# Optimization experiments

Measured on AMD Instinct MI355X. Metric: run time of the kernel, lower is better.

Reference implementation:

```python
import jax, jax.numpy as jnp
import numpy as np

N = 65536        # number of encoding vectors (flattened tokens)
K = 1024         # num_embeddings (codebook size)
D = 128          # embedding_dim
BETA = 0.25


def setup_inputs() -> dict:
    key = jax.random.key(0)
    k_enc, k_cb = jax.random.split(key)
    encoding = jax.random.normal(k_enc, (N, D), dtype=jnp.float32)
    # nn.Embedding weight initialized uniform(-1/K, 1/K)
    codebook = jax.random.uniform(k_cb, (K, D), dtype=jnp.float32,
                                  minval=-1.0 / K, maxval=1.0 / K)
    return {"encoding": encoding, "codebook": codebook}


def reference(encoding, codebook):
    # Nearest codebook entry per row. argmin of L2 distance == argmin of
    # squared distance; expand ||e - w||^2 = ||e||^2 - 2 e.w + ||w||^2.
    # ||e||^2 is constant per row, so it does not affect the argmin.
    scores = (-2.0 * jnp.einsum('nd,kd->nk', encoding, codebook)
              + jnp.sum(codebook * codebook, axis=-1)[None, :])  # [N, K]
    quantized_index = jnp.argmin(scores, axis=-1)                # [N] int
    quantized_embedding = codebook[quantized_index]              # [N, D] gather == onehot @ W

    sg = jax.lax.stop_gradient
    commitment_loss = jnp.mean((sg(quantized_embedding) - encoding) ** 2)
    embedding_loss = jnp.mean((quantized_embedding - sg(encoding)) ** 2)
    vq_loss = commitment_loss * BETA + embedding_loss

    # straight-through estimator
    quantized_st = encoding + sg(quantized_embedding - encoding)

    quantized_index = quantized_index[:, None]  # match torch unsqueeze(1) -> [N, 1]
    return (quantized_index, quantized_st, vq_loss, embedding_loss, commitment_loss)
```

## Files before the change

### kernel.cpp

```cpp
#include <hip/hip_runtime.h>


#define NROWS 65536
#define KCB   1024
#define DIM   128
#define DV    32
#define MSE_DENOM 8388608.0f
#define MARGIN 2.0e-5f
#define FLAGCAP 16384
#define CSCALE   1024.0f
#define CDESCALE 0.0009765625f

#define WS_CNORM_F 256
#define WS_LIST_B  8192
#define WS_PH_B    73728
#define WS_NEEDED  335872

typedef __attribute__((ext_vector_type(16))) float float16v;
typedef _Float16 half8 __attribute__((ext_vector_type(8)));
union U4H8 { uint4 u; half8 h; };
union F4A  { float4 v; float f[4]; };
union HU   { _Float16 f; unsigned short u; };

__device__ __forceinline__ unsigned umn(unsigned a, unsigned b) { return a < b ? a : b; }
__device__ __forceinline__ unsigned umx(unsigned a, unsigned b) { return a > b ? a : b; }
__device__ __forceinline__ float unmap_score(unsigned up) {
  return (up & 0x80000000u) ? __uint_as_float(up ^ 0x80000000u) : __uint_as_float(~up);
}
__device__ __forceinline__ void gload16(const void* g, void* s) {
  __builtin_amdgcn_global_load_lds((const __attribute__((address_space(1))) unsigned int*)g,
                                   (__attribute__((address_space(3))) unsigned int*)s,
                                   16, 0, 0);
}

__global__ __launch_bounds__(256) void vq_prep0(const float* __restrict__ C,
                                                float* __restrict__ wsf) {
  int k = blockIdx.x * 256 + threadIdx.x;
  if (k == 0) { wsf[0] = 0.0f; ((unsigned*)wsf)[1] = 0u; }
  const float4* c4 = (const float4*)C + (size_t)k * DV;
  float s = 0.f;
#pragma unroll 8
  for (int i = 0; i < DV; ++i) {
    float4 v = c4[i];
    s = fmaf(v.x, v.x, s); s = fmaf(v.y, v.y, s);
    s = fmaf(v.z, v.z, s); s = fmaf(v.w, v.w, s);
  }
  wsf[WS_CNORM_F + k] = s;
}

__global__ __launch_bounds__(256) void vq_pack(const float* __restrict__ C,
                                               uint4* __restrict__ PH) {
  int g = blockIdx.x * 256 + threadIdx.x;
  int mt = g >> 9, s = (g >> 6) & 7, l = g & 63;
  int cw = mt * 32 + (l & 31);
  int k0 = s * 16 + (l >> 5) * 8;
  const float* src = C + (size_t)cw * DIM + k0;
  float4 x0 = *(const float4*)src;
  float4 x1 = *(const float4*)(src + 4);
  unsigned h[8];
  {
    float v[8] = {x0.x, x0.y, x0.z, x0.w, x1.x, x1.y, x1.z, x1.w};
#pragma unroll
    for (int j = 0; j < 8; ++j) { HU u; u.f = (_Float16)(CSCALE * v[j]); h[j] = u.u; }
  }
  PH[g] = make_uint4(h[0] | (h[1] << 16), h[2] | (h[3] << 16),
                     h[4] | (h[5] << 16), h[6] | (h[7] << 16));
}

__global__ __launch_bounds__(128, 2) void vq_main5(const float* __restrict__ E,
                                                   const float* __restrict__ C,
                                                   float* __restrict__ wsf,
                                                   float* __restrict__ out) {
  __shared__ uint4 SH[2][512];
  __shared__ __align__(16) float CN[1024];
  __shared__ int BI[64];

  const int tid  = threadIdx.x;
  const int w    = tid >> 6;
  const int l    = tid & 63;
  const int half = l >> 5;
  const int rr   = l & 31;
  const int row0 = blockIdx.x * 64;

  const uint4* PHg = (const uint4*)((const char*)wsf + WS_PH_B);

  {
    const uint4* sh = PHg + tid;
    gload16(sh,       &SH[0][0] + tid);
    gload16(sh + 128, &SH[0][0] + tid + 128);
    gload16(sh + 256, &SH[0][0] + tid + 256);
    gload16(sh + 384, &SH[0][0] + tid + 384);
    const uint4* cn = ((const uint4*)(wsf + WS_CNORM_F)) + tid;
    gload16(cn,       ((uint4*)CN) + tid);
    gload16(cn + 128, ((uint4*)CN) + tid + 128);
  }

  half8 beh[8], bel[8];
  float s2 = 0.f;
  const float* erow = E + (size_t)(row0 + w * 32 + rr) * DIM + half * 8;
#pragma unroll
  for (int s = 0; s < 8; ++s) {
    float4 x0 = *(const float4*)(erow + s * 16);
    float4 x1 = *(const float4*)(erow + s * 16 + 4);
    float v[8] = {x0.x, x0.y, x0.z, x0.w, x1.x, x1.y, x1.z, x1.w};
#pragma unroll
    for (int j = 0; j < 8; ++j) {
      float y = v[j];
      s2 = fmaf(y, y, s2);
      float t = -2.f * y;
      _Float16 hh = (_Float16)t;
      beh[s][j] = hh;
      bel[s][j] = (_Float16)(t - (float)hh);
    }
  }

  asm volatile("s_waitcnt vmcnt(0)" ::: "memory");
  __syncthreads();

  unsigned best = 0xFFFFFFFFu, second = 0xFFFFFFFFu;
  float sc[16];
  int tprev = 0;

#define STAGE_TILE(tn)                                                     \
  {                                                                        \
    const uint4* sh_ = PHg + (size_t)(tn) * 512 + tid;                     \
    uint4* dh_ = &SH[(tn) & 1][0];                                         \
    gload16(sh_,       dh_ + tid);                                         \
    gload16(sh_ + 128, dh_ + tid + 128);                                   \
    gload16(sh_ + 256, dh_ + tid + 256);                                   \
    gload16(sh_ + 384, dh_ + tid + 384);                                   \
  }

#define COMPUTE_TILE(tt, A0, A1)                                           \
  _Pragma("unroll")                                                        \
  for (int s = 0; s < 8; s += 2) {                                         \
    U4H8 h0, h1;                                                           \
    h0.u = SH[(tt) & 1][s * 64 + l];                                       \
    h1.u = SH[(tt) & 1][(s + 1) * 64 + l];                                 \
    A0 = __builtin_amdgcn_mfma_f32_32x32x16_f16(h0.h, beh[s],     A0, 0, 0, 0); \
    A1 = __builtin_amdgcn_mfma_f32_32x32x16_f16(h1.h, beh[s + 1], A1, 0, 0, 0); \
    A0 = __builtin_amdgcn_mfma_f32_32x32x16_f16(h0.h, bel[s],     A0, 0, 0, 0); \
    A1 = __builtin_amdgcn_mfma_f32_32x32x16_f16(h1.h, bel[s + 1], A1, 0, 0, 0); \
  }

#define FOLD_PREV()                                                        \
  {                                                                        \
    const unsigned cwb_ = (unsigned)(tprev * 32 + half * 4);               \
    _Pragma("unroll")                                                      \
    for (int q = 0; q < 4; ++q) {                                          \
      F4A a_; a_.v = *(const float4*)&CN[tprev * 32 + q * 8 + half * 4];   \
      _Pragma("unroll")                                                    \
      for (int i = 0; i < 4; ++i) {                                        \
        float scv_ = fmaf(sc[q * 4 + i], CDESCALE, a_.f[i]);               \
        unsigned u_ = __float_as_uint(scv_);                               \
        u_ ^= ((unsigned)(((int)u_) >> 31)) | 0x80000000u;                 \
        u_ = (u_ & 0xFFFFFC00u) | (cwb_ + (unsigned)(q * 8 + i));          \
        unsigned nb_ = umn(best, u_);                                      \
        second = umn(second, umx(best, u_));                               \
        best = nb_;                                                        \
      }                                                                    \
    }                                                                      \
  }

  {
    STAGE_TILE(1);
    float16v acc0 = {0,0,0,0,0,0,0,0,0,0,0,0,0,0,0,0};
    float16v acc1 = {0,0,0,0,0,0,0,0,0,0,0,0,0,0,0,0};
    COMPUTE_TILE(0, acc0, acc1);
#pragma unroll
    for (int r = 0; r < 16; ++r) sc[r] = acc0[r] + acc1[r];
    tprev = 0;
    asm volatile("s_waitcnt vmcnt(0)" ::: "memory");
    __syncthreads();
  }

  for (int t = 1; t < 32; ++t) {
    if (t < 31) STAGE_TILE(t + 1);
    float16v acc0 = {0,0,0,0,0,0,0,0,0,0,0,0,0,0,0,0};
    float16v acc1 = {0,0,0,0,0,0,0,0,0,0,0,0,0,0,0,0};
    COMPUTE_TILE(t, acc0, acc1);
    FOLD_PREV();
#pragma unroll
    for (int r = 0; r < 16; ++r) sc[r] = acc0[r] + acc1[r];
    tprev = t;
    asm volatile("s_waitcnt vmcnt(0)" ::: "memory");
    __syncthreads();
  }
  FOLD_PREV();

  unsigned ob = (unsigned)__shfl_xor((int)best, 32, 64);
  unsigned os = (unsigned)__shfl_xor((int)second, 32, 64);
  unsigned ns = umn(umn(second, os), umx(best, ob));
  unsigned nb = umn(best, ob);
  float en = s2 + __shfl_xor(s2, 32, 64);

  if (half == 0) {
    const int r = w * 32 + rr;
    int   bi = (int)(nb & 1023u);
    float bv = unmap_score(nb & 0xFFFFFC00u);
    float sv = unmap_score(ns & 0xFFFFFC00u);
    out[row0 + r] = (float)bi;
    BI[r] = bi;
    if (sv - bv < MARGIN) {
      unsigned idx = atomicAdd((unsigned*)wsf + 1, 1u);
      if (idx < FLAGCAP) ((int*)((char*)wsf + WS_LIST_B))[idx] = row0 + r;
    }
    float term = en + bv;
#pragma unroll
    for (int off = 16; off > 0; off >>= 1) term += __shfl_down(term, off);
    if (rr == 0) atomicAdd(wsf, term);
  }
  __syncthreads();

  const float4* C4   = (const float4*)C;
  float4*       out4 = (float4*)out;
#pragma unroll
  for (int it = 0; it < 16; ++it) {
    int flat = it * 128 + tid;
    int r = flat >> 5, d4 = flat & 31;
    out4[(NROWS / 4) + (size_t)(row0 + r) * DV + d4] = C4[(size_t)BI[r] * DV + d4];
  }
#undef STAGE_TILE
#undef COMPUTE_TILE
#undef FOLD_PREV
}

__global__ __launch_bounds__(256) void vq_fix(const float* __restrict__ E,
                                              const float* __restrict__ C,
                                              float* __restrict__ wsf,
                                              float* __restrict__ out) {
  __shared__ float4 eL0[32], eL1[32];
  __shared__ float  sv0[256], sv1[256];
  __shared__ int    si0[256], si1[256];
  __shared__ int    RESi[2];
  const int tid = threadIdx.x;
  const int* list = (const int*)((const char*)wsf + WS_LIST_B);
  int nf = (int)((const unsigned*)wsf)[1];
  if (nf > FLAGCAP) nf = FLAGCAP;
  const float4* E4 = (const float4*)E;
  const float4* C4 = (const float4*)C;
  const float*  cn = wsf + WS_CNORM_F;
  float4* out4 = (float4*)out;

  for (int pair = blockIdx.x; pair * 2 < nf; pair += gridDim.x) {
    const int r0 = list[pair * 2];
    const int r1 = (pair * 2 + 1 < nf) ? list[pair * 2 + 1] : r0;
    if (tid < 32) eL0[tid] = E4[(size_t)r0 * DV + tid];
    else if (tid < 64) eL1[tid - 32] = E4[(size_t)r1 * DV + (tid - 32)];
    __syncthreads();
    float bv0 = 3.0e38f, bv1 = 3.0e38f; int bi0 = 0, bi1 = 0;
#pragma unroll
    for (int j = 0; j < 4; ++j) {
      int k = j * 256 + tid;
      float d0 = 0.f, d1 = 0.f;
#pragma unroll 8
      for (int d4 = 0; d4 < 32; ++d4) {
        float4 c = C4[(size_t)k * DV + d4];
        float4 e0 = eL0[d4], e1 = eL1[d4];
        d0 = fmaf(c.x, e0.x, d0); d0 = fmaf(c.y, e0.y, d0);
        d0 = fmaf(c.z, e0.z, d0); d0 = fmaf(c.w, e0.w, d0);
        d1 = fmaf(c.x, e1.x, d1); d1 = fmaf(c.y, e1.y, d1);
        d1 = fmaf(c.z, e1.z, d1); d1 = fmaf(c.w, e1.w, d1);
      }
      float s0 = fmaf(-2.f, d0, cn[k]);
      float s1 = fmaf(-2.f, d1, cn[k]);
      if (s0 < bv0 || (s0 == bv0 && k < bi0)) { bv0 = s0; bi0 = k; }
      if (s1 < bv1 || (s1 == bv1 && k < bi1)) { bv1 = s1; bi1 = k; }
    }
    sv0[tid] = bv0; si0[tid] = bi0; sv1[tid] = bv1; si1[tid] = bi1;
    __syncthreads();
    if (tid < 64) {
      float v0 = sv0[tid]; int i0 = si0[tid];
      float v1 = sv1[tid]; int i1 = si1[tid];
#pragma unroll
      for (int q = 1; q < 4; ++q) {
        float w0 = sv0[tid + q * 64]; int j0 = si0[tid + q * 64];
        float w1 = sv1[tid + q * 64]; int j1 = si1[tid + q * 64];
        if (w0 < v0 || (w0 == v0 && j0 < i0)) { v0 = w0; i0 = j0; }
        if (w1 < v1 || (w1 == v1 && j1 < i1)) { v1 = w1; i1 = j1; }
      }
#pragma unroll
      for (int off = 32; off > 0; off >>= 1) {
        float w0 = __shfl_down(v0, off); int j0 = __shfl_down(i0, off);
        float w1 = __shfl_down(v1, off); int j1 = __shfl_down(i1, off);
        if (w0 < v0 || (w0 == v0 && j0 < i0)) { v0 = w0; i0 = j0; }
        if (w1 < v1 || (w1 == v1 && j1 < i1)) { v1 = w1; i1 = j1; }
      }
      if (tid == 0) {
        RESi[0] = i0; RESi[1] = i1;
        out[r0] = (float)i0; out[r1] = (float)i1;
      }
    }
    __syncthreads();
    if (tid < 32) out4[(NROWS / 4) + (size_t)r0 * DV + tid] = C4[(size_t)RESi[0] * DV + tid];
    else if (tid < 64) out4[(NROWS / 4) + (size_t)r1 * DV + (tid - 32)] = C4[(size_t)RESi[1] * DV + (tid - 32)];
    __syncthreads();
  }
}

__global__ void vq_final(const float* __restrict__ wsf, float* __restrict__ out) {
  if (threadIdx.x == 0 && blockIdx.x == 0) {
    float mse = wsf[0] / MSE_DENOM;
    out[NROWS + NROWS * DIM + 0] = 1.25f * mse;
    out[NROWS + NROWS * DIM + 1] = mse;
    out[NROWS + NROWS * DIM + 2] = mse;
  }
}

__global__ __launch_bounds__(256) void vq_prep_fb(const float* __restrict__ C,
                                                  float* __restrict__ ws) {
  int k = blockIdx.x * 256 + threadIdx.x;
  if (k == 0) ws[0] = 0.0f;
  const float4* c4 = (const float4*)C + (size_t)k * DV;
  float s = 0.f;
#pragma unroll 8
  for (int i = 0; i < DV; ++i) {
    float4 v = c4[i];
    s = fmaf(v.x, v.x, s); s = fmaf(v.y, v.y, s);
    s = fmaf(v.z, v.z, s); s = fmaf(v.w, v.w, s);
  }
  ws[64 + k] = s;
}

__global__ __launch_bounds__(256) void vq_main_fb(const float* __restrict__ E,
                                                  const float* __restrict__ C,
                                                  const float* __restrict__ cnorm,
                                                  float* __restrict__ out,
                                                  float* __restrict__ lossacc) {
  __shared__ float smem[16384];
  float4* EsV = (float4*)smem;
  float4* CsV = (float4*)(smem + 8192);
  const int tid  = threadIdx.x;
  const int row0 = blockIdx.x * 64;
#pragma unroll
  for (int i = 0; i < 8; ++i) {
    int flat = i * 256 + tid;
    int r = flat >> 5, d4 = flat & 31;
    EsV[r * 32 + (d4 ^ (r & 31))] = ((const float4*)E)[(size_t)(row0 + r) * DV + d4];
  }
  const int tx = tid & 15, ty = tid >> 4;
  int rbase[4], rmask[4];
#pragma unroll
  for (int i = 0; i < 4; ++i) { int r = i * 16 + ty; rbase[i] = r * 32; rmask[i] = r & 31; }
  float bestv[4]; int besti[4];
#pragma unroll
  for (int i = 0; i < 4; ++i) { bestv[i] = 3.0e38f; besti[i] = 0; }
  for (int ch = 0; ch < 16; ++ch) {
    const int k0 = ch * 64;
    __syncthreads();
#pragma unroll
    for (int i = 0; i < 8; ++i) {
      int flat = i * 256 + tid;
      int k = flat >> 5, d4 = flat & 31;
      CsV[k * 32 + (d4 ^ (k & 31))] = ((const float4*)C)[(size_t)(k0 + k) * DV + d4];
    }
    __syncthreads();
    float acc[4][4] = {};
#pragma unroll 8
    for (int d4 = 0; d4 < DV; ++d4) {
      float4 a[4], b[4];
#pragma unroll
      for (int i = 0; i < 4; ++i) a[i] = EsV[rbase[i] + (d4 ^ rmask[i])];
#pragma unroll
      for (int j = 0; j < 4; ++j) { int k = j * 16 + tx; b[j] = CsV[k * 32 + (d4 ^ (k & 31))]; }
#pragma unroll
      for (int i = 0; i < 4; ++i)
#pragma unroll
        for (int j = 0; j < 4; ++j) {
          acc[i][j] = fmaf(a[i].x, b[j].x, acc[i][j]);
          acc[i][j] = fmaf(a[i].y, b[j].y, acc[i][j]);
          acc[i][j] = fmaf(a[i].z, b[j].z, acc[i][j]);
          acc[i][j] = fmaf(a[i].w, b[j].w, acc[i][j]);
        }
    }
#pragma unroll
    for (int j = 0; j < 4; ++j) {
      int kg = k0 + j * 16 + tx;
      float cnv = cnorm[kg];
#pragma unroll
      for (int i = 0; i < 4; ++i) {
        float s = fmaf(-2.0f, acc[i][j], cnv);
        if (s < bestv[i] || (s == bestv[i] && kg < besti[i])) { bestv[i] = s; besti[i] = kg; }
      }
    }
  }
  float* Rv = smem + 8192;
  int*   Ri = (int*)(smem + 9216);
  int*   BIf = (int*)(smem + 10240);
  __syncthreads();
#pragma unroll
  for (int i = 0; i < 4; ++i) {
    int r = i * 16 + ty;
    Rv[r * 16 + tx] = bestv[i];
    Ri[r * 16 + tx] = besti[i];
  }
  __syncthreads();
  if (tid < 64) {
    const int r = tid;
    float bv = Rv[r * 16]; int bi = Ri[r * 16];
#pragma unroll
    for (int t = 1; t < 16; ++t) {
      float v = Rv[r * 16 + t]; int ii = Ri[r * 16 + t];
      if (v < bv || (v == bv && ii < bi)) { bv = v; bi = ii; }
    }
    float en = 0.f;
#pragma unroll 8
    for (int d4 = 0; d4 < DV; ++d4) {
      float4 v = EsV[r * 32 + (d4 ^ (r & 31))];
      en = fmaf(v.x, v.x, en); en = fmaf(v.y, v.y, en);
      en = fmaf(v.z, v.z, en); en = fmaf(v.w, v.w, en);
    }
    out[row0 + r] = (float)bi;
    BIf[r] = bi;
    float blocksum = en + bv;
#pragma unroll
    for (int off = 32; off > 0; off >>= 1) blocksum += __shfl_down(blocksum, off);
    if (tid == 0) atomicAdd(lossacc, blocksum);
  }
  __syncthreads();
  const float4* C4   = (const float4*)C;
  float4*       out4 = (float4*)out;
  for (int flat = tid; flat < 64 * DV; flat += 256) {
    int r = flat >> 5, d4 = flat & 31;
    out4[(NROWS / 4) + (size_t)(row0 + r) * DV + d4] = C4[(size_t)BIf[r] * DV + d4];
  }
}

__global__ void vq_final_fb(const float* __restrict__ ws, float* __restrict__ out) {
  if (threadIdx.x == 0 && blockIdx.x == 0) {
    float mse = ws[0] / MSE_DENOM;
    out[NROWS + NROWS * DIM + 0] = 1.25f * mse;
    out[NROWS + NROWS * DIM + 1] = mse;
    out[NROWS + NROWS * DIM + 2] = mse;
  }
}

extern "C" void kernel_launch(void* const* d_in, const int* in_sizes, int n_in,
                              void* d_out, int out_size, void* d_ws, size_t ws_size,
                              hipStream_t stream) {
  const float* E = (const float*)d_in[0];
  const float* C = (const float*)d_in[1];
  float* out = (float*)d_out;
  float* wsf = (float*)d_ws;

  if (ws_size >= (size_t)WS_NEEDED) {
    uint4* PH = (uint4*)((char*)d_ws + WS_PH_B);
    vq_prep0<<<4, 256, 0, stream>>>(C, wsf);
    vq_pack<<<64, 256, 0, stream>>>(C, PH);
    vq_main5<<<NROWS / 64, 128, 0, stream>>>(E, C, wsf, out);
    vq_fix<<<512, 256, 0, stream>>>(E, C, wsf, out);
    vq_final<<<1, 64, 0, stream>>>(wsf, out);
  } else {
    vq_prep_fb<<<4, 256, 0, stream>>>(C, wsf);
    vq_main_fb<<<NROWS / 64, 256, 0, stream>>>(E, C, wsf + 64, out, wsf);
    vq_final_fb<<<1, 64, 0, stream>>>(wsf, out);
  }
}
```

Measured before the change: 167.0 us.

## Drop fp16 lo-split MFMA pass, double tile width, batch four rows in fix

The main kernel now converts the encoding to a single fp16 term instead of a hi+lo split, which halves the number of MFMA instructions. It also stages two 32-codeword tiles per iteration, so there are half as many barriers and fold phases, but the previous fold-overlap pipelining is gone. To make up for the lower precision, the candidate margin widens, and the exact fp32 fix kernel processes four flagged rows per block with wave-level shuffle reductions. The risk is that more rows get flagged for the slower exact fallback pass.

```diff
diff --git a/kernel.cpp b/kernel.cpp
--- a/kernel.cpp
+++ b/kernel.cpp
@@ -6,7 +6,7 @@
 #define DIM   128
 #define DV    32
 #define MSE_DENOM 8388608.0f
-#define MARGIN 2.0e-5f
+#define MARGIN 3.0e-5f
 #define FLAGCAP 16384
 #define CSCALE   1024.0f
 #define CDESCALE 0.0009765625f
@@ -33,9 +33,9 @@
                                    16, 0, 0);
 }
 
-__global__ __launch_bounds__(256) void vq_prep0(const float* __restrict__ C,
-                                                float* __restrict__ wsf) {
-  int k = blockIdx.x * 256 + threadIdx.x;
+__global__ __launch_bounds__(64) void vq_prep0(const float* __restrict__ C,
+                                               float* __restrict__ wsf) {
+  int k = blockIdx.x * 64 + threadIdx.x;
   if (k == 0) { wsf[0] = 0.0f; ((unsigned*)wsf)[1] = 0u; }
   const float4* c4 = (const float4*)C + (size_t)k * DV;
   float s = 0.f;
@@ -67,11 +67,11 @@
                      h[4] | (h[5] << 16), h[6] | (h[7] << 16));
 }
 
-__global__ __launch_bounds__(128, 2) void vq_main5(const float* __restrict__ E,
+__global__ __launch_bounds__(128, 2) void vq_main6(const float* __restrict__ E,
                                                    const float* __restrict__ C,
                                                    float* __restrict__ wsf,
                                                    float* __restrict__ out) {
-  __shared__ uint4 SH[2][512];
+  __shared__ uint4 SH[2][1024];
   __shared__ __align__(16) float CN[1024];
   __shared__ int BI[64];
 
@@ -86,16 +86,15 @@
 
   {
     const uint4* sh = PHg + tid;
-    gload16(sh,       &SH[0][0] + tid);
-    gload16(sh + 128, &SH[0][0] + tid + 128);
-    gload16(sh + 256, &SH[0][0] + tid + 256);
-    gload16(sh + 384, &SH[0][0] + tid + 384);
+#pragma unroll
+    for (int k = 0; k < 8; ++k)
+      gload16(sh + k * 128, &SH[0][0] + tid + k * 128);
     const uint4* cn = ((const uint4*)(wsf + WS_CNORM_F)) + tid;
     gload16(cn,       ((uint4*)CN) + tid);
     gload16(cn + 128, ((uint4*)CN) + tid + 128);
   }
 
-  half8 beh[8], bel[8];
+  half8 beh[8];
   float s2 = 0.f;
   const float* erow = E + (size_t)(row0 + w * 32 + rr) * DIM + half * 8;
 #pragma unroll
@@ -107,10 +106,7 @@
     for (int j = 0; j < 8; ++j) {
       float y = v[j];
       s2 = fmaf(y, y, s2);
-      float t = -2.f * y;
-      _Float16 hh = (_Float16)t;
-      beh[s][j] = hh;
-      bel[s][j] = (_Float16)(t - (float)hh);
+      beh[s][j] = (_Float16)(-2.f * y);
     }
   }
 
@@ -118,75 +114,59 @@
   __syncthreads();
 
   unsigned best = 0xFFFFFFFFu, second = 0xFFFFFFFFu;
-  float sc[16];
-  int tprev = 0;
-
-#define STAGE_TILE(tn)                                                     \
-  {                                                                        \
-    const uint4* sh_ = PHg + (size_t)(tn) * 512 + tid;                     \
-    uint4* dh_ = &SH[(tn) & 1][0];                                         \
-    gload16(sh_,       dh_ + tid);                                         \
-    gload16(sh_ + 128, dh_ + tid + 128);                                   \
-    gload16(sh_ + 256, dh_ + tid + 256);                                   \
-    gload16(sh_ + 384, dh_ + tid + 384);                                   \
-  }
-
-#define COMPUTE_TILE(tt, A0, A1)                                           \
-  _Pragma("unroll")                                                        \
-  for (int s = 0; s < 8; s += 2) {                                         \
-    U4H8 h0, h1;                                                           \
-    h0.u = SH[(tt) & 1][s * 64 + l];                                       \
-    h1.u = SH[(tt) & 1][(s + 1) * 64 + l];                                 \
-    A0 = __builtin_amdgcn_mfma_f32_32x32x16_f16(h0.h, beh[s],     A0, 0, 0, 0); \
-    A1 = __builtin_amdgcn_mfma_f32_32x32x16_f16(h1.h, beh[s + 1], A1, 0, 0, 0); \
-    A0 = __builtin_amdgcn_mfma_f32_32x32x16_f16(h0.h, bel[s],     A0, 0, 0, 0); \
-    A1 = __builtin_amdgcn_mfma_f32_32x32x16_f16(h1.h, bel[s + 1], A1, 0, 0, 0); \
-  }
-
-#define FOLD_PREV()                                                        \
-  {                                                                        \
-    const unsigned cwb_ = (unsigned)(tprev * 32 + half * 4);               \
-    _Pragma("unroll")                                                      \
-    for (int q = 0; q < 4; ++q) {                                          \
-      F4A a_; a_.v = *(const float4*)&CN[tprev * 32 + q * 8 + half * 4];   \
-      _Pragma("unroll")                                                    \
-      for (int i = 0; i < 4; ++i) {                                        \
-        float scv_ = fmaf(sc[q * 4 + i], CDESCALE, a_.f[i]);               \
-        unsigned u_ = __float_as_uint(scv_);                               \
-        u_ ^= ((unsigned)(((int)u_) >> 31)) | 0x80000000u;                 \
-        u_ = (u_ & 0xFFFFFC00u) | (cwb_ + (unsigned)(q * 8 + i));          \
-        unsigned nb_ = umn(best, u_);                                      \
-        second = umn(second, umx(best, u_));                               \
-        best = nb_;                                                        \
-      }                                                                    \
-    }                                                                      \
-  }
-
-  {
-    STAGE_TILE(1);
-    float16v acc0 = {0,0,0,0,0,0,0,0,0,0,0,0,0,0,0,0};
-    float16v acc1 = {0,0,0,0,0,0,0,0,0,0,0,0,0,0,0,0};
-    COMPUTE_TILE(0, acc0, acc1);
-#pragma unroll
-    for (int r = 0; r < 16; ++r) sc[r] = acc0[r] + acc1[r];
-    tprev = 0;
+
+  for (int t = 0; t < 16; ++t) {
+    const int b = t & 1;
+    if (t < 15) {
+      const uint4* sh = PHg + (size_t)(t + 1) * 1024 + tid;
+      uint4* dh = &SH[b ^ 1][0];
+#pragma unroll
+      for (int k = 0; k < 8; ++k)
+        gload16(sh + k * 128, dh + tid + k * 128);
+    }
+
+    float16v a0 = {0,0,0,0,0,0,0,0,0,0,0,0,0,0,0,0};
+    float16v a1 = {0,0,0,0,0,0,0,0,0,0,0,0,0,0,0,0};
+    float16v b0 = {0,0,0,0,0,0,0,0,0,0,0,0,0,0,0,0};
+    float16v b1 = {0,0,0,0,0,0,0,0,0,0,0,0,0,0,0,0};
+#pragma unroll
+    for (int s = 0; s < 8; s += 2) {
+      U4H8 hA0, hA1, hB0, hB1;
+      hA0.u = SH[b][s * 64 + l];
+      hA1.u = SH[b][(s + 1) * 64 + l];
+      hB0.u = SH[b][512 + s * 64 + l];
+      hB1.u = SH[b][512 + (s + 1) * 64 + l];
+      a0 = __builtin_amdgcn_mfma_f32_32x32x16_f16(hA0.h, beh[s],     a0, 0, 0, 0);
+      a1 = __builtin_amdgcn_mfma_f32_32x32x16_f16(hA1.h, beh[s + 1], a1, 0, 0, 0);
+      b0 = __builtin_amdgcn_mfma_f32_32x32x16_f16(hB0.h, beh[s],     b0, 0, 0, 0);
+      b1 = __builtin_amdgcn_mfma_f32_32x32x16_f16(hB1.h, beh[s + 1], b1, 0, 0, 0);
+    }
+
+#pragma unroll
+    for (int tt = 0; tt < 2; ++tt) {
+      const int tg = t * 2 + tt;
+      const unsigned cwb = (unsigned)(tg * 32 + half * 4);
+#pragma unroll
+      for (int q = 0; q < 4; ++q) {
+        F4A a; a.v = *(const float4*)&CN[tg * 32 + q * 8 + half * 4];
+#pragma unroll
+        for (int i = 0; i < 4; ++i) {
+          float acc = tt ? (b0[q * 4 + i] + b1[q * 4 + i])
+                         : (a0[q * 4 + i] + a1[q * 4 + i]);
+          float sc = fmaf(acc, CDESCALE, a.f[i]);
+          unsigned u = __float_as_uint(sc);
+          u ^= ((unsigned)(((int)u) >> 31)) | 0x80000000u;
+          u = (u & 0xFFFFFC00u) | (cwb + (unsigned)(q * 8 + i));
+          unsigned nb = umn(best, u);
+          second = umn(second, umx(best, u));
+          best = nb;
+        }
+      }
+    }
+
     asm volatile("s_waitcnt vmcnt(0)" ::: "memory");
     __syncthreads();
   }
-
-  for (int t = 1; t < 32; ++t) {
-    if (t < 31) STAGE_TILE(t + 1);
-    float16v acc0 = {0,0,0,0,0,0,0,0,0,0,0,0,0,0,0,0};
-    float16v acc1 = {0,0,0,0,0,0,0,0,0,0,0,0,0,0,0,0};
-    COMPUTE_TILE(t, acc0, acc1);
-    FOLD_PREV();
-#pragma unroll
-    for (int r = 0; r < 16; ++r) sc[r] = acc0[r] + acc1[r];
-    tprev = t;
-    asm volatile("s_waitcnt vmcnt(0)" ::: "memory");
-    __syncthreads();
-  }
-  FOLD_PREV();
 
   unsigned ob = (unsigned)__shfl_xor((int)best, 32, 64);
   unsigned os = (unsigned)__shfl_xor((int)second, 32, 64);
@@ -220,20 +200,19 @@
     int r = flat >> 5, d4 = flat & 31;
     out4[(NROWS / 4) + (size_t)(row0 + r) * DV + d4] = C4[(size_t)BI[r] * DV + d4];
   }
-#undef STAGE_TILE
-#undef COMPUTE_TILE
-#undef FOLD_PREV
 }
 
 __global__ __launch_bounds__(256) void vq_fix(const float* __restrict__ E,
                                               const float* __restrict__ C,
                                               float* __restrict__ wsf,
                                               float* __restrict__ out) {
-  __shared__ float4 eL0[32], eL1[32];
-  __shared__ float  sv0[256], sv1[256];
-  __shared__ int    si0[256], si1[256];
-  __shared__ int    RESi[2];
+  __shared__ float4 eL[4][32];
+  __shared__ float  RV[4][4];
+  __shared__ int    RI[4][4];
+  __shared__ int    RESi[4];
   const int tid = threadIdx.x;
+  const int wv  = tid >> 6;
+  const int ln  = tid & 63;
   const int* list = (const int*)((const char*)wsf + WS_LIST_B);
   int nf = (int)((const unsigned*)wsf)[1];
   if (nf > FLAGCAP) nf = FLAGCAP;
@@ -242,58 +221,75 @@
   const float*  cn = wsf + WS_CNORM_F;
   float4* out4 = (float4*)out;
 
-  for (int pair = blockIdx.x; pair * 2 < nf; pair += gridDim.x) {
-    const int r0 = list[pair * 2];
-    const int r1 = (pair * 2 + 1 < nf) ? list[pair * 2 + 1] : r0;
-    if (tid < 32) eL0[tid] = E4[(size_t)r0 * DV + tid];
-    else if (tid < 64) eL1[tid - 32] = E4[(size_t)r1 * DV + (tid - 32)];
-    __syncthreads();
-    float bv0 = 3.0e38f, bv1 = 3.0e38f; int bi0 = 0, bi1 = 0;
+  for (int g = blockIdx.x; g * 4 < nf; g += gridDim.x) {
+    const int base = g * 4;
+    if (tid < 128) {
+      int r = tid >> 5, d4 = tid & 31;
+      int R = (base + r < nf) ? list[base + r] : list[base];
+      eL[r][d4] = E4[(size_t)R * DV + d4];
+    }
+    __syncthreads();
+    float bv[4] = {3.0e38f, 3.0e38f, 3.0e38f, 3.0e38f};
+    int   bi[4] = {0, 0, 0, 0};
 #pragma unroll
     for (int j = 0; j < 4; ++j) {
       int k = j * 256 + tid;
-      float d0 = 0.f, d1 = 0.f;
-#pragma unroll 8
+      float d0 = 0.f, d1 = 0.f, d2 = 0.f, d3 = 0.f;
+#pragma unroll 4
       for (int d4 = 0; d4 < 32; ++d4) {
         float4 c = C4[(size_t)k * DV + d4];
-        float4 e0 = eL0[d4], e1 = eL1[d4];
+        float4 e0 = eL[0][d4], e1 = eL[1][d4], e2 = eL[2][d4], e3 = eL[3][d4];
         d0 = fmaf(c.x, e0.x, d0); d0 = fmaf(c.y, e0.y, d0);
         d0 = fmaf(c.z, e0.z, d0); d0 = fmaf(c.w, e0.w, d0);
         d1 = fmaf(c.x, e1.x, d1); d1 = fmaf(c.y, e1.y, d1);
         d1 = fmaf(c.z, e1.z, d1); d1 = fmaf(c.w, e1.w, d1);
-      }
-      float s0 = fmaf(-2.f, d0, cn[k]);
-      float s1 = fmaf(-2.f, d1, cn[k]);
-      if (s0 < bv0 || (s0 == bv0 && k < bi0)) { bv0 = s0; bi0 = k; }
-      if (s1 < bv1 || (s1 == bv1 && k < bi1)) { bv1 = s1; bi1 = k; }
-    }
-    sv0[tid] = bv0; si0[tid] = bi0; sv1[tid] = bv1; si1[tid] = bi1;
-    __syncthreads();
-    if (tid < 64) {
-      float v0 = sv0[tid]; int i0 = si0[tid];
-      float v1 = sv1[tid]; int i1 = si1[tid];
+        d2 = fmaf(c.x, e2.x, d2); d2 = fmaf(c.y, e2.y, d2);
+        d2 = fmaf(c.z, e2.z, d2); d2 = fmaf(c.w, e2.w, d2);
+        d3 = fmaf(c.x, e3.x, d3); d3 = fmaf(c.y, e3.y, d3);
+        d3 = fmaf(c.z, e3.z, d3); d3 = fmaf(c.w, e3.w, d3);
+      }
+      float cnk = cn[k];
+      float s0 = fmaf(-2.f, d0, cnk);
+      float s1 = fmaf(-2.f, d1, cnk);
+      float s2 = fmaf(-2.f, d2, cnk);
+      float s3 = fmaf(-2.f, d3, cnk);
+      if (s0 < bv[0] || (s0 == bv[0] && k < bi[0])) { bv[0] = s0; bi[0] = k; }
+      if (s1 < bv[1] || (s1 == bv[1] && k < bi[1])) { bv[1] = s1; bi[1] = k; }
+      if (s2 < bv[2] || (s2 == bv[2] && k < bi[2])) { bv[2] = s2; bi[2] = k; }
+      if (s3 < bv[3] || (s3 == bv[3] && k < bi[3])) { bv[3] = s3; bi[3] = k; }
+    }
+#pragma unroll
+    for (int off = 32; off > 0; off >>= 1) {
+#pragma unroll
+      for (int r = 0; r < 4; ++r) {
+        float wv_ = __shfl_down(bv[r], off);
+        int   ji  = __shfl_down(bi[r], off);
+        if (wv_ < bv[r] || (wv_ == bv[r] && ji < bi[r])) { bv[r] = wv_; bi[r] = ji; }
+      }
+    }
+    if (ln == 0) {
+#pragma unroll
+      for (int r = 0; r < 4; ++r) { RV[wv][r] = bv[r]; RI[wv][r] = bi[r]; }
+    }
+    __syncthreads();
+    if (tid < 4) {
+      float v = RV[0][tid]; int i = RI[0][tid];
 #pragma unroll
       for (int q = 1; q < 4; ++q) {
-        float w0 = sv0[tid + q * 64]; int j0 = si0[tid + q * 64];
-        float w1 = sv1[tid + q * 64]; int j1 = si1[tid + q * 64];
-        if (w0 < v0 || (w0 == v0 && j0 < i0)) { v0 = w0; i0 = j0; }
-        if (w1 < v1 || (w1 == v1 && j1 < i1)) { v1 = w1; i1 = j1; }
-      }
-#pragma unroll
-      for (int off = 32; off > 0; off >>= 1) {
-        float w0 = __shfl_down(v0, off); int j0 = __shfl_down(i0, off);
-        float w1 = __shfl_down(v1, off); int j1 = __shfl_down(i1, off);
-        if (w0 < v0 || (w0 == v0 && j0 < i0)) { v0 = w0; i0 = j0; }
-        if (w1 < v1 || (w1 == v1 && j1 < i1)) { v1 = w1; i1 = j1; }
-      }
-      if (tid == 0) {
-        RESi[0] = i0; RESi[1] = i1;
-        out[r0] = (float)i0; out[r1] = (float)i1;
-      }
-    }
-    __syncthreads();
-    if (tid < 32) out4[(NROWS / 4) + (size_t)r0 * DV + tid] = C4[(size_t)RESi[0] * DV + tid];
-    else if (tid < 64) out4[(NROWS / 4) + (size_t)r1 * DV + (tid - 32)] = C4[(size_t)RESi[1] * DV + (tid - 32)];
+        float vv = RV[q][tid]; int ii = RI[q][tid];
+        if (vv < v || (vv == v && ii < i)) { v = vv; i = ii; }
+      }
+      RESi[tid] = i;
+      if (base + tid < nf) out[list[base + tid]] = (float)i;
+    }
+    __syncthreads();
+    if (tid < 128) {
+      int r = tid >> 5, d4 = tid & 31;
+      if (base + r < nf) {
+        int R = list[base + r];
+        out4[(NROWS / 4) + (size_t)R * DV + d4] = C4[(size_t)RESi[r] * DV + d4];
+      }
+    }
     __syncthreads();
   }
 }
@@ -445,10 +441,10 @@
 
   if (ws_size >= (size_t)WS_NEEDED) {
     uint4* PH = (uint4*)((char*)d_ws + WS_PH_B);
-    vq_prep0<<<4, 256, 0, stream>>>(C, wsf);
+    vq_prep0<<<16, 64, 0, stream>>>(C, wsf);
     vq_pack<<<64, 256, 0, stream>>>(C, PH);
-    vq_main5<<<NROWS / 64, 128, 0, stream>>>(E, C, wsf, out);
-    vq_fix<<<512, 256, 0, stream>>>(E, C, wsf, out);
+    vq_main6<<<NROWS / 64, 128, 0, stream>>>(E, C, wsf, out);
+    vq_fix<<<256, 256, 0, stream>>>(E, C, wsf, out);
     vq_final<<<1, 64, 0, stream>>>(wsf, out);
   } else {
     vq_prep_fb<<<4, 256, 0, stream>>>(C, wsf);
```

Measured after the change: 166.8 us. No clear change (-0.1%).
